# Performance work log

Measured on AMD Instinct MI355X. Metric: run time of the kernel, lower is better.

Reference implementation:

```python
import jax, jax.numpy as jnp
import numpy as np

B, S_PREV, E, H, LOW = 8, 4095, 2048, 16, 512
HD = E // H  # 128
ROPE_BASE = 10000.0


def _rope(x, pos):
    # x: [..., S, d], pos: [S]; half-split rotary
    d = x.shape[-1]
    half = d // 2
    inv_freq = 1.0 / (ROPE_BASE ** (jnp.arange(half, dtype=jnp.float32) / half))
    ang = pos.astype(jnp.float32)[:, None] * inv_freq  # [S, half]
    cos, sin = jnp.cos(ang), jnp.sin(ang)
    x1, x2 = x[..., :half], x[..., half:]
    return jnp.concatenate([x1 * cos - x2 * sin, x1 * sin + x2 * cos], axis=-1)


def setup_inputs() -> dict:
    key = jax.random.key(0)
    ks = jax.random.split(key, 10)

    def w(k, *shape):
        return jax.random.normal(k, shape, dtype=jnp.float32) * (1.0 / np.float32(np.sqrt(shape[0])))

    return {
        "x": jax.random.normal(ks[0], (B, 1, E), dtype=jnp.float32),
        "ckv_cache": jax.random.normal(ks[1], (B, S_PREV, LOW), dtype=jnp.float32),
        "kr_cache": jax.random.normal(ks[2], (B, S_PREV, HD), dtype=jnp.float32),
        "Wdq": w(ks[3], E, E),
        "Wuq": w(ks[4], E, E),
        "Wqr": w(ks[5], E, HD),
        "Wdkv": w(ks[6], E, LOW),
        "Wkr": w(ks[7], E, HD),
        "fused_upsample": w(ks[8], LOW, 2 * E),
        "Wo": w(ks[9], E, E),
    }


def reference(x, ckv_cache, kr_cache, Wdq, Wuq, Wqr, Wdkv, Wkr, fused_upsample, Wo):
    Bx = x.shape[0]
    # update compressed KV caches with the current token
    ckv = jnp.concatenate([ckv_cache, x @ Wdkv], axis=1)            # [B,S,LOW]
    kr = jnp.concatenate([kr_cache, x @ Wkr], axis=1)               # [B,S,HD]
    S = ckv.shape[1]
    up = ckv @ fused_upsample                                       # [B,S,2E]
    k_up, v = up[..., :E], up[..., E:]
    Kc = k_up.reshape(Bx, S, H, HD).transpose(0, 2, 1, 3)           # [B,H,S,HD]
    Kr = _rope(kr, jnp.arange(S))                                   # [B,S,HD] shared rope-K
    Kr = jnp.broadcast_to(Kr[:, None], (Bx, H, S, HD))
    v = v.reshape(Bx, S, H, HD).transpose(0, 2, 1, 3)               # [B,H,S,HD]
    # query path
    Cq = x @ Wdq                                                    # [B,1,E]
    Qc = (Cq @ Wuq).reshape(Bx, 1, H, HD).transpose(0, 2, 1, 3)     # [B,H,1,HD]
    Qr = _rope(Cq @ Wqr, jnp.arange(S - 1, S))                      # [B,1,HD] at last pos
    Qr = jnp.broadcast_to(Qr[:, None], (Bx, H, 1, HD))
    q = jnp.concatenate([Qc, Qr], axis=-1)                          # [B,H,1,2HD]
    k = jnp.concatenate([Kc, Kr], axis=-1)                          # [B,H,S,2HD]
    scores = jnp.einsum('bhqd,bhkd->bhqk', q, k) / np.float32(np.sqrt(2 * HD))
    attn = jax.nn.softmax(scores, axis=-1)
    o = jnp.einsum('bhqk,bhkd->bhqd', attn, v)                      # [B,H,1,HD]
    out = o.transpose(0, 2, 1, 3).reshape(Bx, 1, E) @ Wo            # [B,1,E]
    return out
```

## Files before the change

kernel.cpp:

```cpp
#include <hip/hip_runtime.h>
#include <hip/hip_bf16.h>

#define B_ 8
#define SPREV 4095
#define S_ 4096
#define E_ 2048
#define H_ 16
#define HD_ 128
#define LOW_ 512
#define NCH 64
#define CHK 64
#define L2INV 0.207620506f

typedef short s8v __attribute__((ext_vector_type(8)));
typedef float f4v __attribute__((ext_vector_type(4)));

__device__ __forceinline__ short f2bf_s(float f) {
  return (short)__bfloat16_as_ushort(__float2bfloat16(f));
}
__device__ __forceinline__ float bf2f(unsigned short h) {
  union { unsigned u; float f; } v; v.u = ((unsigned)h) << 16;
  return v.f;
}

__global__ __launch_bounds__(256) void init_kernel(float* __restrict__ ws_pre,
                                                   float* __restrict__ out) {
  int i = blockIdx.x * 256 + threadIdx.x;
  if (i < 55296) ws_pre[i] = 0.f;
  else if (i < 71680) out[i - 55296] = 0.f;
}

__global__ __launch_bounds__(128) void matvec8(
    const float* __restrict__ x, int K,
    const float* __restrict__ W0, int N0, float* __restrict__ o0,
    const float* __restrict__ W1, int N1, float* __restrict__ o1,
    const float* __restrict__ W2, int N2, float* __restrict__ o2)
{
  int cb = blockIdx.x;
  int nb0 = N0 >> 7, nb1 = N1 >> 7;
  const float* W; float* o; int N, colbase;
  if (cb < nb0)            { W = W0; o = o0; N = N0; colbase = cb << 7; }
  else if (cb < nb0 + nb1) { W = W1; o = o1; N = N1; colbase = (cb - nb0) << 7; }
  else                     { W = W2; o = o2; N = N2; colbase = (cb - nb0 - nb1) << 7; }
  int col = colbase + threadIdx.x;
  int k0 = blockIdx.y * 32;
  float acc[B_];
  #pragma unroll
  for (int b = 0; b < B_; ++b) acc[b] = 0.f;
  const float* Wp = W + (size_t)k0 * N + col;
  #pragma unroll 8
  for (int k = 0; k < 32; ++k) {
    float wv = Wp[(size_t)k * N];
    #pragma unroll
    for (int b = 0; b < B_; ++b)
      acc[b] = fmaf(x[b * K + k0 + k], wv, acc[b]);
  }
  #pragma unroll
  for (int b = 0; b < B_; ++b) atomicAdd(&o[b * N + col], acc[b]);
}

__global__ __launch_bounds__(256) void qeff_kernel(
    const float* __restrict__ Qc, const float* __restrict__ FU,
    unsigned short* __restrict__ qeff)
{
  int bx = blockIdx.x, b = blockIdx.y, t = threadIdx.x;
  int h = bx >> 2, lq = bx & 3;
  int g = t >> 4, li = t & 15;
  __shared__ float qs[HD_];
  if (t < 128) qs[t] = Qc[b * E_ + h * HD_ + t];
  __syncthreads();
  f4v q0 = *(const f4v*)&qs[li * 8];
  f4v q1 = *(const f4v*)&qs[li * 8 + 4];
  #pragma unroll 2
  for (int p = 0; p < 8; ++p) {
    int l = lq * 128 + p * 16 + g;
    const f4v* w4 = (const f4v*)(FU + (size_t)l * (2 * E_) + h * HD_ + li * 8);
    f4v w0 = w4[0], w1 = w4[1];
    float a = w0[0]*q0[0] + w0[1]*q0[1] + w0[2]*q0[2] + w0[3]*q0[3]
            + w1[0]*q1[0] + w1[1]*q1[1] + w1[2]*q1[2] + w1[3]*q1[3];
    a += __shfl_xor(a, 1); a += __shfl_xor(a, 2);
    a += __shfl_xor(a, 4); a += __shfl_xor(a, 8);
    if (li == 0) qeff[(size_t)(b * H_ + h) * LOW_ + l] = (unsigned short)f2bf_s(a);
  }
}

__global__ __launch_bounds__(512) void attn_kernel(
    const float* __restrict__ ckv_cache, const float* __restrict__ ckv_new,
    const unsigned short* __restrict__ qeff,
    const float* __restrict__ kr_cache, const float* __restrict__ kr_new,
    const float* __restrict__ qr_pre,
    unsigned short* __restrict__ acc_part, float* __restrict__ m_part,
    float* __restrict__ l_part)
{
  int chunk = blockIdx.x, b = blockIdx.y;
  int tid = threadIdx.x;
  int w = tid >> 6, lane = tid & 63;
  int kg = lane >> 4, l16 = lane & 15;
  __shared__ float S_lds[2][16 * 64];
  __shared__ unsigned short P_lds[16 * 64];
  __shared__ float qr_sh[128];
  __shared__ float rope_lds[64];

  if (tid < 64) {
    float invf = exp2f(-L2INV * (float)tid);
    float x1 = qr_pre[b * HD_ + tid], x2 = qr_pre[b * HD_ + 64 + tid];
    float sn, cs; sincosf(4095.0f * invf, &sn, &cs);
    qr_sh[tid]      = x1 * cs - x2 * sn;
    qr_sh[64 + tid] = x1 * sn + x2 * cs;
  }
  __syncthreads();

  {
    int kh = w >> 2;
    int s_loc = (w & 3) * 16 + l16;
    int s = chunk * CHK + s_loc;
    const float* crow = (s == S_ - 1) ? (ckv_new + b * LOW_)
                                      : (ckv_cache + ((size_t)b * SPREV + s) * LOW_);
    f4v acc0 = {0.f, 0.f, 0.f, 0.f};
    f4v acc1 = {0.f, 0.f, 0.f, 0.f};
    const s8v* qf = (const s8v*)(qeff + (size_t)(b * H_ + l16) * LOW_);
    #pragma unroll
    for (int bt = 0; bt < 2; ++bt) {
      f4v c0_[4], c1_[4];
      s8v aq[4];
      #pragma unroll
      for (int u = 0; u < 4; ++u) {
        int kk = kh * 8 + bt * 4 + u;
        const float* cp = crow + kk * 32 + kg * 8;
        c0_[u] = *(const f4v*)cp;
        c1_[u] = *(const f4v*)(cp + 4);
        aq[u] = qf[kk * 4 + kg];
      }
      #pragma unroll
      for (int u = 0; u < 4; ++u) {
        s8v bv;
        bv[0]=f2bf_s(c0_[u][0]); bv[1]=f2bf_s(c0_[u][1]);
        bv[2]=f2bf_s(c0_[u][2]); bv[3]=f2bf_s(c0_[u][3]);
        bv[4]=f2bf_s(c1_[u][0]); bv[5]=f2bf_s(c1_[u][1]);
        bv[6]=f2bf_s(c1_[u][2]); bv[7]=f2bf_s(c1_[u][3]);
        if (u & 1)
          acc1 = __builtin_amdgcn_mfma_f32_16x16x32_bf16(aq[u], bv, acc1, 0, 0, 0);
        else
          acc0 = __builtin_amdgcn_mfma_f32_16x16x32_bf16(aq[u], bv, acc0, 0, 0, 0);
      }
    }
    #pragma unroll
    for (int r = 0; r < 4; ++r) {
      int h = kg * 4 + r;
      S_lds[kh][h * 64 + (s_loc ^ ((h & 7) << 2))] = acc0[r] + acc1[r];
    }
    if (w < 4) {
      const float* krp = (s == S_ - 1) ? (kr_new + b * HD_)
                                       : (kr_cache + ((size_t)b * SPREV + s) * HD_);
      float fs = (float)s;
      float rdot = 0.f;
      #pragma unroll
      for (int q = 0; q < 4; ++q) {
        int j = kg * 16 + q * 4;
        f4v x1 = *(const f4v*)&krp[j];
        f4v x2 = *(const f4v*)&krp[64 + j];
        f4v qa = *(const f4v*)&qr_sh[j];
        f4v qb = *(const f4v*)&qr_sh[64 + j];
        #pragma unroll
        for (int k2 = 0; k2 < 4; ++k2) {
          float invf = exp2f(-L2INV * (float)(j + k2));
          float sn, cs; sincosf(fs * invf, &sn, &cs);
          rdot += qa[k2] * (x1[k2] * cs - x2[k2] * sn)
                + qb[k2] * (x1[k2] * sn + x2[k2] * cs);
        }
      }
      rdot += __shfl_xor(rdot, 16);
      rdot += __shfl_xor(rdot, 32);
      if (kg == 0) rope_lds[s_loc] = rdot;
    }
  }
  __syncthreads();

  {
    int half = lane >> 5;
    int h = w * 2 + half;
    int sl = lane & 31;
    int s0 = sl * 2;
    int c2 = (h & 7) << 2;
    float v0 = (S_lds[0][h * 64 + (s0 ^ c2)] + S_lds[1][h * 64 + (s0 ^ c2)]
                + rope_lds[s0]) * 0.0625f;
    float v1 = (S_lds[0][h * 64 + ((s0 + 1) ^ c2)] + S_lds[1][h * 64 + ((s0 + 1) ^ c2)]
                + rope_lds[s0 + 1]) * 0.0625f;
    float m = fmaxf(v0, v1);
    m = fmaxf(m, __shfl_xor(m, 1));  m = fmaxf(m, __shfl_xor(m, 2));
    m = fmaxf(m, __shfl_xor(m, 4));  m = fmaxf(m, __shfl_xor(m, 8));
    m = fmaxf(m, __shfl_xor(m, 16));
    float e0 = expf(v0 - m), e1 = expf(v1 - m);
    float lsum = e0 + e1;
    lsum += __shfl_xor(lsum, 1);  lsum += __shfl_xor(lsum, 2);
    lsum += __shfl_xor(lsum, 4);  lsum += __shfl_xor(lsum, 8);
    lsum += __shfl_xor(lsum, 16);
    unsigned pk = (unsigned)(unsigned short)f2bf_s(e0) |
                  ((unsigned)(unsigned short)f2bf_s(e1) << 16);
    *(unsigned*)&P_lds[h * 64 + (s0 ^ ((h & 7) << 3))] = pk;
    if (sl == 0) {
      int idx = (b * NCH + chunk) * H_ + h;
      m_part[idx] = m;
      l_part[idx] = lsum;
    }
  }
  __syncthreads();

  {
    s8v pa[2];
    const float* rp[2][8];
    #pragma unroll
    for (int kt = 0; kt < 2; ++kt) {
      int so = kt * 32 + kg * 8;
      pa[kt] = *(const s8v*)&P_lds[l16 * 64 + (so ^ ((l16 & 7) << 3))];
      #pragma unroll
      for (int i = 0; i < 8; ++i) {
        int s = chunk * CHK + so + i;
        rp[kt][i] = (s == S_ - 1) ? (ckv_new + b * LOW_)
                                  : (ckv_cache + ((size_t)b * SPREV + s) * LOW_);
      }
    }
    f4v oa[4];
    #pragma unroll
    for (int nt = 0; nt < 4; ++nt) oa[nt] = {0.f, 0.f, 0.f, 0.f};
    #pragma unroll
    for (int nt = 0; nt < 4; ++nt) {
      int l = w * 64 + nt * 16 + l16;
      float vb0[8], vb1[8];
      #pragma unroll
      for (int i = 0; i < 8; ++i) { vb0[i] = rp[0][i][l]; vb1[i] = rp[1][i][l]; }
      s8v bv0, bv1;
      #pragma unroll
      for (int i = 0; i < 8; ++i) {
        bv0[i] = f2bf_s(vb0[i]);
        bv1[i] = f2bf_s(vb1[i]);
      }
      oa[nt] = __builtin_amdgcn_mfma_f32_16x16x32_bf16(pa[0], bv0, oa[nt], 0, 0, 0);
      oa[nt] = __builtin_amdgcn_mfma_f32_16x16x32_bf16(pa[1], bv1, oa[nt], 0, 0, 0);
    }
    size_t base = (size_t)(b * NCH + chunk) * H_;
    #pragma unroll
    for (int nt = 0; nt < 4; ++nt) {
      int l = w * 64 + nt * 16 + l16;
      #pragma unroll
      for (int r = 0; r < 4; ++r) {
        int h = kg * 4 + r;
        acc_part[(base + h) * LOW_ + l] = (unsigned short)f2bf_s(oa[nt][r]);
      }
    }
  }
}

__global__ __launch_bounds__(128) void reduce_proj_kernel(
    const float* __restrict__ m_part, const float* __restrict__ l_part,
    const unsigned short* __restrict__ acc_part, const float* __restrict__ FU,
    float* __restrict__ o_heads)
{
  int h = blockIdx.x, b = blockIdx.y, lz = blockIdx.z, t = threadIdx.x;
  __shared__ float wls[NCH];
  __shared__ float Linv_s;
  __shared__ float pa0[128], pa1[128];
  __shared__ float wl_sh[64];
  if (t < 64) {
    float mc = m_part[(b * NCH + t) * H_ + h];
    float M = mc;
    #pragma unroll
    for (int d = 1; d < 64; d <<= 1) M = fmaxf(M, __shfl_xor(M, d));
    float wc = expf(mc - M);
    float L = l_part[(b * NCH + t) * H_ + h] * wc;
    #pragma unroll
    for (int d = 1; d < 64; d <<= 1) L += __shfl_xor(L, d);
    wls[t] = wc;
    if (t == 0) Linv_s = 1.0f / L;
  }
  __syncthreads();
  {
    int p = t & 31, ch = t >> 5;
    int l0 = lz * 64 + p * 2;
    float a0 = 0.f, a1 = 0.f;
    const unsigned short* ap =
        acc_part + ((size_t)(b * NCH + ch * 16) * H_ + h) * LOW_ + l0;
    #pragma unroll 4
    for (int c = 0; c < 16; ++c) {
      unsigned pk = *(const unsigned*)(ap + (size_t)c * H_ * LOW_);
      float wc = wls[ch * 16 + c];
      a0 = fmaf(bf2f((unsigned short)(pk & 0xffffu)), wc, a0);
      a1 = fmaf(bf2f((unsigned short)(pk >> 16)),     wc, a1);
    }
    pa0[t] = a0; pa1[t] = a1;
  }
  __syncthreads();
  if (t < 32) {
    float inv = Linv_s;
    float s0 = pa0[t] + pa0[t + 32] + pa0[t + 64] + pa0[t + 96];
    float s1 = pa1[t] + pa1[t + 32] + pa1[t + 64] + pa1[t + 96];
    wl_sh[t * 2]     = s0 * inv;
    wl_sh[t * 2 + 1] = s1 * inv;
  }
  __syncthreads();
  {
    float a = 0.f;
    const float* fp = FU + (size_t)(lz * 64) * (2 * E_) + E_ + h * HD_ + t;
    #pragma unroll 4
    for (int l = 0; l < 64; ++l)
      a = fmaf(wl_sh[l], fp[(size_t)l * (2 * E_)], a);
    atomicAdd(&o_heads[(b * H_ + h) * HD_ + t], a);
  }
}

extern "C" void kernel_launch(void* const* d_in, const int* in_sizes, int n_in,
                              void* d_out, int out_size, void* d_ws, size_t ws_size,
                              hipStream_t stream)
{
  const float* x    = (const float*)d_in[0];
  const float* ckvc = (const float*)d_in[1];
  const float* krc  = (const float*)d_in[2];
  const float* Wdq  = (const float*)d_in[3];
  const float* Wuq  = (const float*)d_in[4];
  const float* Wqr  = (const float*)d_in[5];
  const float* Wdkv = (const float*)d_in[6];
  const float* Wkr  = (const float*)d_in[7];
  const float* FU   = (const float*)d_in[8];
  const float* Wo   = (const float*)d_in[9];
  float* out = (float*)d_out;

  char* ws = (char*)d_ws;
  float* Cq             = (float*)(ws + 0);
  float* Qc             = (float*)(ws + 65536);
  float* qr_pre         = (float*)(ws + 131072);
  float* ckvn           = (float*)(ws + 135168);
  float* krn            = (float*)(ws + 151552);
  float* o_heads        = (float*)(ws + 155648);
  unsigned short* qeff  = (unsigned short*)(ws + 221184);
  float* m_part         = (float*)(ws + 352256);
  float* l_part         = (float*)(ws + 385024);
  unsigned short* accp  = (unsigned short*)(ws + 417792);

  init_kernel<<<280, 256, 0, stream>>>((float*)ws, out);

  matvec8<<<dim3(21, 64), 128, 0, stream>>>(x, E_, Wdq, E_, Cq,
                                            Wdkv, LOW_, ckvn, Wkr, HD_, krn);
  matvec8<<<dim3(17, 64), 128, 0, stream>>>(Cq, E_, Wuq, E_, Qc,
                                            Wqr, HD_, qr_pre,
                                            (const float*)nullptr, 0, (float*)nullptr);
  qeff_kernel<<<dim3(64, 8), 256, 0, stream>>>(Qc, FU, qeff);
  attn_kernel<<<dim3(64, 8), 512, 0, stream>>>(ckvc, ckvn, qeff, krc, krn,
                                               qr_pre, accp, m_part, l_part);
  reduce_proj_kernel<<<dim3(16, 8, 8), 128, 0, stream>>>(m_part, l_part, accp,
                                                         FU, o_heads);
  matvec8<<<dim3(16, 64), 128, 0, stream>>>(o_heads, E_, Wo, E_, out,
                                            (const float*)nullptr, 0, (float*)nullptr,
                                            (const float*)nullptr, 0, (float*)nullptr);
}
```

Baseline: 82.74 us.

## Prefetch ckv cache into L2/MALL from extra blocks in earlier kernels

Extra blocks are added to the second matvec and the qeff kernel. They read the ckv cache (8×4095×512 floats, about 67 MB) in two halves and discard the values, so the data is warm in the large last-level cache before the attention kernel runs. This overlaps part of the attention kernel's main memory traffic with the small, latency-bound projection kernels. The cost is extra HBM traffic competing with those kernels. It only helps if the cache hierarchy keeps the data until attention runs.

```diff
diff --git a/kernel.cpp b/kernel.cpp
--- a/kernel.cpp
+++ b/kernel.cpp
@@ -11,6 +11,8 @@
 #define NCH 64
 #define CHK 64
 #define L2INV 0.207620506f
+#define CKV4_N 4193280
+#define CKV4_H 2096640
 
 typedef short s8v __attribute__((ext_vector_type(8)));
 typedef float f4v __attribute__((ext_vector_type(4)));
@@ -21,6 +23,9 @@
 __device__ __forceinline__ float bf2f(unsigned short h) {
   union { unsigned u; float f; } v; v.u = ((unsigned)h) << 16;
   return v.f;
+}
+__device__ __forceinline__ void sink_f4(f4v v) {
+  asm volatile("" :: "v"(v[0]), "v"(v[1]), "v"(v[2]), "v"(v[3]));
 }
 
 __global__ __launch_bounds__(256) void init_kernel(float* __restrict__ ws_pre,
@@ -34,10 +39,21 @@
     const float* __restrict__ x, int K,
     const float* __restrict__ W0, int N0, float* __restrict__ o0,
     const float* __restrict__ W1, int N1, float* __restrict__ o1,
-    const float* __restrict__ W2, int N2, float* __restrict__ o2)
+    const float* __restrict__ W2, int N2, float* __restrict__ o2,
+    const float* __restrict__ pf4, int pf_base4, int pf_n4, int pf_nb)
 {
   int cb = blockIdx.x;
-  int nb0 = N0 >> 7, nb1 = N1 >> 7;
+  int nb0 = N0 >> 7, nb1 = N1 >> 7, nb2 = N2 >> 7;
+  int nbsum = nb0 + nb1 + nb2;
+  if (cb >= nbsum) {
+    int seg = (cb - nbsum) * gridDim.y + blockIdx.y;
+    int ftid = seg * 128 + threadIdx.x;
+    const f4v* p4 = (const f4v*)pf4;
+    for (int i = pf_base4 + ftid; i < pf_base4 + pf_n4; i += pf_nb * 128) {
+      f4v v = p4[i]; sink_f4(v);
+    }
+    return;
+  }
   const float* W; float* o; int N, colbase;
   if (cb < nb0)            { W = W0; o = o0; N = N0; colbase = cb << 7; }
   else if (cb < nb0 + nb1) { W = W1; o = o1; N = N1; colbase = (cb - nb0) << 7; }
@@ -61,9 +77,19 @@
 
 __global__ __launch_bounds__(256) void qeff_kernel(
     const float* __restrict__ Qc, const float* __restrict__ FU,
-    unsigned short* __restrict__ qeff)
+    unsigned short* __restrict__ qeff,
+    const float* __restrict__ pf4, int pf_base4, int pf_n4)
 {
   int bx = blockIdx.x, b = blockIdx.y, t = threadIdx.x;
+  if (bx >= 64) {
+    int seg = (bx - 64) * 8 + b;
+    int ftid = seg * 256 + t;
+    const f4v* p4 = (const f4v*)pf4;
+    for (int i = pf_base4 + ftid; i < pf_base4 + pf_n4; i += 512 * 256) {
+      f4v v = p4[i]; sink_f4(v);
+    }
+    return;
+  }
   int h = bx >> 2, lq = bx & 3;
   int g = t >> 4, li = t & 15;
   __shared__ float qs[HD_];
@@ -339,16 +365,20 @@
   init_kernel<<<280, 256, 0, stream>>>((float*)ws, out);
 
   matvec8<<<dim3(21, 64), 128, 0, stream>>>(x, E_, Wdq, E_, Cq,
-                                            Wdkv, LOW_, ckvn, Wkr, HD_, krn);
-  matvec8<<<dim3(17, 64), 128, 0, stream>>>(Cq, E_, Wuq, E_, Qc,
+                                            Wdkv, LOW_, ckvn, Wkr, HD_, krn,
+                                            (const float*)nullptr, 0, 0, 1);
+  matvec8<<<dim3(34, 64), 128, 0, stream>>>(Cq, E_, Wuq, E_, Qc,
                                             Wqr, HD_, qr_pre,
-                                            (const float*)nullptr, 0, (float*)nullptr);
-  qeff_kernel<<<dim3(64, 8), 256, 0, stream>>>(Qc, FU, qeff);
+                                            (const float*)nullptr, 0, (float*)nullptr,
+                                            ckvc, 0, CKV4_H, 1088);
+  qeff_kernel<<<dim3(128, 8), 256, 0, stream>>>(Qc, FU, qeff,
+                                                ckvc, CKV4_H, CKV4_H);
   attn_kernel<<<dim3(64, 8), 512, 0, stream>>>(ckvc, ckvn, qeff, krc, krn,
                                                qr_pre, accp, m_part, l_part);
   reduce_proj_kernel<<<dim3(16, 8, 8), 128, 0, stream>>>(m_part, l_part, accp,
                                                          FU, o_heads);
   matvec8<<<dim3(16, 64), 128, 0, stream>>>(o_heads, E_, Wo, E_, out,
                                             (const float*)nullptr, 0, (float*)nullptr,
-                                            (const float*)nullptr, 0, (float*)nullptr);
-}
+                                            (const float*)nullptr, 0, (float*)nullptr,
+                                            (const float*)nullptr, 0, 0, 1);
+}
```

After: 85.97 us. 1.04x slower.
